# Kernel optimization log

Hardware: AMD Instinct MI355X
Metric: run time of the kernel (lower is better)

## Reference

```python
import jax, jax.numpy as jnp
import numpy as np
from jax import lax

B = 2; H = 32; W = 32; C = 384
NH = 12; NG = 6; KK = 7; STRIDE = 1; ORF = 2.0
CG = C // NG; HC = C // NH; GH = NH // NG; HID = 4 * C
EPS = 1e-5


def layernorm(x, w, b):
    mu = jnp.mean(x, axis=-1, keepdims=True)
    var = jnp.mean((x - mu) ** 2, axis=-1, keepdims=True)
    return (x - mu) * lax.rsqrt(var + EPS) * w + b


def ref_points(Hk, Wk):
    # normalized reference grid in (-1,1), ordering (y, x) as in _get_ref_points
    ry = ((jnp.arange(Hk, dtype=jnp.float32) + 0.5) / Hk) * 2.0 - 1.0
    rx = ((jnp.arange(Wk, dtype=jnp.float32) + 0.5) / Wk) * 2.0 - 1.0
    return jnp.stack(jnp.meshgrid(ry, rx, indexing='ij'), axis=-1)  # (Hk, Wk, 2)


def grid_sample(img, grid):
    # torch F.grid_sample: bilinear, align_corners=True, padding_mode='zeros'
    # img: (N, Cc, Hi, Wi); grid: (N, ..., 2) with (x, y) in [-1, 1]
    N, Cc, Hi, Wi = img.shape
    out_shape = grid.shape[1:-1]
    g = grid.reshape(N, -1, 2)
    x = (g[..., 0] + 1.0) * 0.5 * (Wi - 1)
    y = (g[..., 1] + 1.0) * 0.5 * (Hi - 1)
    x0 = jnp.floor(x); y0 = jnp.floor(y)
    wx1 = x - x0; wy1 = y - y0
    flat = img.reshape(N, Cc, Hi * Wi)
    M = g.shape[1]
    def gather(ix, iy, wgt):
        valid = (ix >= 0) & (ix <= Wi - 1) & (iy >= 0) & (iy <= Hi - 1)
        idx = (jnp.clip(iy, 0, Hi - 1) * Wi + jnp.clip(ix, 0, Wi - 1)).astype(jnp.int32)
        vals = jnp.take_along_axis(flat, jnp.broadcast_to(idx[:, None, :], (N, Cc, M)), axis=2)
        return vals * (wgt * valid.astype(img.dtype))[:, None, :]
    out = (gather(x0, y0, (1 - wx1) * (1 - wy1))
           + gather(x0 + 1, y0, wx1 * (1 - wy1))
           + gather(x0, y0 + 1, (1 - wx1) * wy1)
           + gather(x0 + 1, y0 + 1, wx1 * wy1))
    return out.reshape((N, Cc) + out_shape)


def setup_inputs() -> dict:
    ks = jax.random.split(jax.random.key(0), 16)
    n = lambda k, s, sc=0.02: jax.random.normal(k, s, jnp.float32) * sc
    return dict(
        x=jax.random.normal(ks[0], (B, H * W, C), jnp.float32),
        norm1_w=jnp.ones((C,), jnp.float32), norm1_b=jnp.zeros((C,), jnp.float32),
        wq=n(ks[1], (C, C)), bq=jnp.zeros((C,), jnp.float32),
        wk=n(ks[2], (C, C)), bk=jnp.zeros((C,), jnp.float32),
        wv=n(ks[3], (C, C)), bv=jnp.zeros((C,), jnp.float32),
        wo=n(ks[4], (C, C)), bo=jnp.zeros((C,), jnp.float32),
        off_dw_w=n(ks[5], (CG, 1, KK, KK)), off_dw_b=jnp.zeros((CG,), jnp.float32),
        off_ln_w=jnp.ones((CG,), jnp.float32), off_ln_b=jnp.zeros((CG,), jnp.float32),
        off_pw_w=n(ks[6], (2, CG)),
        rpe_table=n(ks[7], (NH, 2 * H - 1, 2 * W - 1), 0.01),
        norm2_w=jnp.ones((C,), jnp.float32), norm2_b=jnp.zeros((C,), jnp.float32),
        fc1_w=n(ks[8], (HID, C)), fc1_b=jnp.zeros((HID,), jnp.float32),
        fc2_w=n(ks[9], (C, HID)), fc2_b=jnp.zeros((C,), jnp.float32),
    )


def reference(x, norm1_w, norm1_b, wq, bq, wk, bk, wv, bv, wo, bo,
              off_dw_w, off_dw_b, off_ln_w, off_ln_b, off_pw_w, rpe_table,
              norm2_w, norm2_b, fc1_w, fc1_b, fc2_w, fc2_b):
    Bx, L, Cx = x.shape
    shortcut = x
    xn = layernorm(x, norm1_w, norm1_b)
    xi = xn.reshape(Bx, H, W, Cx).transpose(0, 3, 1, 2)  # (B, C, H, W)

    # proj_q (1x1 conv)
    q = jnp.einsum('bchw,dc->bdhw', xi, wq) + bq[None, :, None, None]

    # offset network on per-group channels
    q_off = q.reshape(Bx * NG, CG, H, W)
    o = lax.conv_general_dilated(q_off, off_dw_w, (STRIDE, STRIDE),
                                 [(KK // 2, KK // 2), (KK // 2, KK // 2)],
                                 dimension_numbers=('NCHW', 'OIHW', 'NCHW'),
                                 feature_group_count=CG) + off_dw_b[None, :, None, None]
    o = layernorm(o.transpose(0, 2, 3, 1), off_ln_w, off_ln_b)  # (Bg, Hk, Wk, CG)
    o = jax.nn.gelu(o, approximate=False)
    offset = jnp.einsum('bhwc,pc->bphw', o, off_pw_w)  # (Bg, 2, Hk, Wk)
    Hk, Wk = offset.shape[2], offset.shape[3]
    ns = Hk * Wk
    orange = jnp.array([1.0 / Hk, 1.0 / Wk], jnp.float32).reshape(1, 2, 1, 1)
    offset = jnp.tanh(offset) * orange * ORF
    offset = offset.transpose(0, 2, 3, 1)  # (Bg, Hk, Wk, 2) (y, x)
    pos = offset + ref_points(Hk, Wk)[None]  # offset_range_factor >= 0 branch

    # deformable sampling of the (normed) feature map
    xs = grid_sample(xi.reshape(Bx * NG, CG, H, W), pos[..., ::-1])  # (Bg, CG, Hk, Wk)
    xs = xs.reshape(Bx, Cx, 1, ns)

    k = (jnp.einsum('bcxn,dc->bdxn', xs, wk) + bk[None, :, None, None]).reshape(Bx * NH, HC, ns)
    v = (jnp.einsum('bcxn,dc->bdxn', xs, wv) + bv[None, :, None, None]).reshape(Bx * NH, HC, ns)
    q_ = q.reshape(Bx * NH, HC, H * W)

    attn = jnp.einsum('bcm,bcn->bmn', q_, k) * (HC ** -0.5)  # (B*NH, HW, ns)

    # continuous relative position bias via grid_sample on rpe_table
    rpe = jnp.broadcast_to(rpe_table[None], (Bx, NH, 2 * H - 1, 2 * W - 1)).reshape(
        Bx * NG, GH, 2 * H - 1, 2 * W - 1)
    qg = ref_points(H, W).reshape(H * W, 2)[None]  # (1, HW, 2)
    disp = (qg[:, :, None, :] - pos.reshape(Bx * NG, ns, 2)[:, None, :, :]) * 0.5  # (Bg, HW, ns, 2)
    bias = grid_sample(rpe, disp[..., ::-1])  # (Bg, GH, HW, ns)
    attn = attn + bias.reshape(Bx * NH, H * W, ns)

    attn = jax.nn.softmax(attn, axis=2)
    out = jnp.einsum('bmn,bcn->bcm', attn, v).reshape(Bx, Cx, H, W)
    y = jnp.einsum('bchw,dc->bdhw', out, wo) + bo[None, :, None, None]
    y = y.transpose(0, 2, 3, 1).reshape(Bx, L, Cx)

    x2 = shortcut + y
    h = layernorm(x2, norm2_w, norm2_b)
    h = jax.nn.gelu(h @ fc1_w.T + fc1_b, approximate=False) @ fc2_w.T + fc2_b
    return x2 + h
```

## Files before the change

kernel.cpp:

```cpp
#include <hip/hip_runtime.h>
#include <math.h>

#define Bc 2
#define Hh 32
#define Ww 32
#define Cc 384
#define NHc 12
#define NGc 6
#define CGc 64
#define HCc 32
#define GHc 2
#define HIDc 1536
#define Lc 1024
#define NSc 1024
#define BGc 12

typedef float f32x4 __attribute__((ext_vector_type(4)));
typedef short bf16x8 __attribute__((ext_vector_type(8)));

__device__ __forceinline__ float gelu_f(float v) {
    return 0.5f * v * (1.f + erff(v * 0.70710678118654752440f));
}

__device__ __forceinline__ unsigned short f2bf(float f) {
    unsigned u = __float_as_uint(f);
    u = (u + 0x7FFF + ((u >> 16) & 1)) >> 16;
    return (unsigned short)u;
}

__device__ __forceinline__ float bf2f(unsigned short u) {
    return __uint_as_float((unsigned)u << 16);
}

__global__ __launch_bounds__(128) void ln_kernel(
    const float* __restrict__ x, const float* __restrict__ w,
    const float* __restrict__ b, unsigned short* __restrict__ out)
{
    __shared__ float l1[2], l2[2];
    int row = blockIdx.x;
    int t = threadIdx.x;
    const float* xr = x + (size_t)row * Cc;
    float v0 = xr[t], v1 = xr[t + 128], v2 = xr[t + 256];
    float s = v0 + v1 + v2;
    #pragma unroll
    for (int o = 32; o; o >>= 1) s += __shfl_down(s, o);
    if ((t & 63) == 0) l1[t >> 6] = s;
    __syncthreads();
    float mu = (l1[0] + l1[1]) * (1.f / Cc);
    float d0 = v0 - mu, d1 = v1 - mu, d2 = v2 - mu;
    float q = d0 * d0 + d1 * d1 + d2 * d2;
    #pragma unroll
    for (int o = 32; o; o >>= 1) q += __shfl_down(q, o);
    if ((t & 63) == 0) l2[t >> 6] = q;
    __syncthreads();
    float rstd = rsqrtf((l2[0] + l2[1]) * (1.f / Cc) + 1e-5f);
    unsigned short* orow = out + (size_t)row * Cc;
    orow[t]       = f2bf(d0 * rstd * w[t]       + b[t]);
    orow[t + 128] = f2bf(d1 * rstd * w[t + 128] + b[t + 128]);
    orow[t + 256] = f2bf(d2 * rstd * w[t + 256] + b[t + 256]);
}

__global__ __launch_bounds__(256) void cast6_kernel(
    const float* __restrict__ wq, const float* __restrict__ wk,
    const float* __restrict__ wv, const float* __restrict__ wo,
    const float* __restrict__ f1, const float* __restrict__ f2,
    unsigned short* __restrict__ dq, unsigned short* __restrict__ dk,
    unsigned short* __restrict__ dv, unsigned short* __restrict__ d_o,
    unsigned short* __restrict__ d1, unsigned short* __restrict__ d2)
{
    int bid = blockIdx.x;
    const float* s; unsigned short* d; int base;
    if (bid < 144)       { s = wq; d = dq;  base = bid; }
    else if (bid < 288)  { s = wk; d = dk;  base = bid - 144; }
    else if (bid < 432)  { s = wv; d = dv;  base = bid - 288; }
    else if (bid < 576)  { s = wo; d = d_o; base = bid - 432; }
    else if (bid < 1152) { s = f1; d = d1;  base = bid - 576; }
    else                 { s = f2; d = d2;  base = bid - 1152; }
    int i = base * 1024 + threadIdx.x * 4;
    float4 v = *(const float4*)(s + i);
    ushort4 u;
    u.x = f2bf(v.x); u.y = f2bf(v.y); u.z = f2bf(v.z); u.w = f2bf(v.w);
    *(ushort4*)(d + i) = u;
}

template<int EPI>
__global__ __launch_bounds__(256) void mfma_gemm(
    const unsigned short* __restrict__ A, const unsigned short* __restrict__ W,
    const float* __restrict__ bias, const float* __restrict__ res,
    void* __restrict__ out1, void* __restrict__ out2, int M, int N, int K)
{
    int w = threadIdx.x >> 6, l = threadIdx.x & 63;
    int col = l & 15, quad = l >> 4;
    int mb = blockIdx.x * 64 + w * 16;
    int n0 = blockIdx.y * 32;
    const unsigned short* Ap = A + (size_t)(mb + col) * K + quad * 8;
    const unsigned short* Wp0 = W + (size_t)(n0 + col) * K + quad * 8;
    const unsigned short* Wp1 = W + (size_t)(n0 + 16 + col) * K + quad * 8;
    f32x4 acc[2] = {};
    #pragma unroll 4
    for (int k0 = 0; k0 < K; k0 += 32) {
        bf16x8 af = *(const bf16x8*)(Ap + k0);
        bf16x8 w0 = *(const bf16x8*)(Wp0 + k0);
        bf16x8 w1 = *(const bf16x8*)(Wp1 + k0);
        acc[0] = __builtin_amdgcn_mfma_f32_16x16x32_bf16(af, w0, acc[0], 0, 0, 0);
        acc[1] = __builtin_amdgcn_mfma_f32_16x16x32_bf16(af, w1, acc[1], 0, 0, 0);
    }
    int bb = mb >> 10, l0 = (mb & 1023) + quad * 4;
    #pragma unroll
    for (int ch = 0; ch < 2; ch++) {
        int n = n0 + ch * 16 + col;
        float bv = bias[n];
        if (EPI == 3) {
            unsigned short u0 = f2bf(acc[ch][0] + bv);
            unsigned short u1 = f2bf(acc[ch][1] + bv);
            unsigned short u2 = f2bf(acc[ch][2] + bv);
            unsigned short u3 = f2bf(acc[ch][3] + bv);
            ushort4 qv = {u0, u1, u2, u3};
            *(ushort4*)&((unsigned short*)out1)[((size_t)(bb * Cc + n)) * Lc + l0] = qv;
            unsigned short* q2 = (unsigned short*)out2;
            size_t base = (((size_t)(bb * NHc + (n >> 5))) * Lc + l0) * 32 + (n & 31);
            q2[base] = u0; q2[base + 32] = u1; q2[base + 64] = u2; q2[base + 96] = u3;
        } else {
            #pragma unroll
            for (int r = 0; r < 4; r++) {
                size_t m = mb + quad * 4 + r;
                float v = acc[ch][r] + bv;
                if (EPI == 1)
                    ((unsigned short*)out1)[m * N + n] = f2bf(gelu_f(v));
                else
                    ((float*)out1)[m * N + n] = v + res[m * N + n];
            }
        }
    }
}

__global__ __launch_bounds__(256) void mfma_kv(
    const unsigned short* __restrict__ A, const unsigned short* __restrict__ Wk,
    const unsigned short* __restrict__ Wv, const float* __restrict__ bk,
    const float* __restrict__ bv, unsigned short* __restrict__ kout,
    unsigned short* __restrict__ vout, int M, int K)
{
    int w = threadIdx.x >> 6, l = threadIdx.x & 63;
    int col = l & 15, quad = l >> 4;
    int mb = blockIdx.x * 64 + w * 16;
    int n0 = blockIdx.y * 32;
    const unsigned short* Ap = A + (size_t)(mb + col) * K + quad * 8;
    const unsigned short* Wk0 = Wk + (size_t)(n0 + col) * K + quad * 8;
    const unsigned short* Wk1 = Wk + (size_t)(n0 + 16 + col) * K + quad * 8;
    const unsigned short* Wv0 = Wv + (size_t)(n0 + col) * K + quad * 8;
    const unsigned short* Wv1 = Wv + (size_t)(n0 + 16 + col) * K + quad * 8;
    f32x4 ak[2] = {}, av[2] = {};
    #pragma unroll 4
    for (int k0 = 0; k0 < K; k0 += 32) {
        bf16x8 af = *(const bf16x8*)(Ap + k0);
        bf16x8 k0f = *(const bf16x8*)(Wk0 + k0);
        bf16x8 k1f = *(const bf16x8*)(Wk1 + k0);
        bf16x8 v0f = *(const bf16x8*)(Wv0 + k0);
        bf16x8 v1f = *(const bf16x8*)(Wv1 + k0);
        ak[0] = __builtin_amdgcn_mfma_f32_16x16x32_bf16(af, k0f, ak[0], 0, 0, 0);
        ak[1] = __builtin_amdgcn_mfma_f32_16x16x32_bf16(af, k1f, ak[1], 0, 0, 0);
        av[0] = __builtin_amdgcn_mfma_f32_16x16x32_bf16(af, v0f, av[0], 0, 0, 0);
        av[1] = __builtin_amdgcn_mfma_f32_16x16x32_bf16(af, v1f, av[1], 0, 0, 0);
    }
    int bb = mb >> 10, l0 = (mb & 1023) + quad * 4;
    #pragma unroll
    for (int ch = 0; ch < 2; ch++) {
        int n = n0 + ch * 16 + col;
        float bkv = bk[n], bvv = bv[n];
        #pragma unroll
        for (int r = 0; r < 4; r++)
            kout[(size_t)(mb + quad * 4 + r) * Cc + n] = f2bf(ak[ch][r] + bkv);
        ushort4 u;
        u.x = f2bf(av[ch][0] + bvv); u.y = f2bf(av[ch][1] + bvv);
        u.z = f2bf(av[ch][2] + bvv); u.w = f2bf(av[ch][3] + bvv);
        *(ushort4*)&vout[((size_t)(bb * Cc + n)) * NSc + l0] = u;
    }
}

__global__ __launch_bounds__(256) void dwconv_kernel(
    const unsigned short* __restrict__ q, const float* __restrict__ wdw,
    const float* __restrict__ bdw, float* __restrict__ o_dw)
{
    int cg = blockIdx.x, bg = blockIdx.y;
    int b = bg / NGc, g = bg % NGc;
    __shared__ float wk_s[49];
    __shared__ float img[1024];
    const unsigned short* qp = q + (size_t)(b * Cc + g * CGc + cg) * Lc;
    if (threadIdx.x < 49) wk_s[threadIdx.x] = wdw[cg * 49 + threadIdx.x];
    #pragma unroll
    for (int i = 0; i < 4; i++)
        img[threadIdx.x + i * 256] = bf2f(qp[threadIdx.x + i * 256]);
    __syncthreads();
    float bias = bdw[cg];
    #pragma unroll
    for (int i = 0; i < 4; i++) {
        int hw = threadIdx.x + i * 256;
        int y = hw >> 5, xx = hw & 31;
        float acc = bias;
        #pragma unroll
        for (int ky = 0; ky < 7; ky++) {
            int yy = y + ky - 3;
            if (yy < 0 || yy > 31) continue;
            #pragma unroll
            for (int kx = 0; kx < 7; kx++) {
                int x2 = xx + kx - 3;
                if (x2 < 0 || x2 > 31) continue;
                acc += img[yy * 32 + x2] * wk_s[ky * 7 + kx];
            }
        }
        o_dw[(size_t)(bg * CGc + cg) * Lc + hw] = acc;
    }
}

__global__ __launch_bounds__(256) void offset_kernel(
    const float* __restrict__ o_dw, const float* __restrict__ lnw,
    const float* __restrict__ lnb, const float* __restrict__ pw,
    float* __restrict__ pos)
{
    int hw = blockIdx.x * 4 + (threadIdx.x >> 6);
    int bg = blockIdx.y;
    int cg = threadIdx.x & 63;
    float v = o_dw[(size_t)(bg * CGc + cg) * Lc + hw];
    float s = v;
    #pragma unroll
    for (int o = 32; o; o >>= 1) s += __shfl_down(s, o);
    s = __shfl(s, 0, 64);
    float mu = s * (1.f / CGc);
    float d = v - mu;
    float q2 = d * d;
    #pragma unroll
    for (int o = 32; o; o >>= 1) q2 += __shfl_down(q2, o);
    q2 = __shfl(q2, 0, 64);
    float rstd = rsqrtf(q2 * (1.f / CGc) + 1e-5f);
    float t = d * rstd * lnw[cg] + lnb[cg];
    float gl = gelu_f(t);
    float sy = gl * pw[cg];
    float sx = gl * pw[CGc + cg];
    #pragma unroll
    for (int o = 32; o; o >>= 1) {
        sy += __shfl_down(sy, o);
        sx += __shfl_down(sx, o);
    }
    if (cg == 0) {
        float offy = tanhf(sy) * 0.0625f;
        float offx = tanhf(sx) * 0.0625f;
        int y = hw >> 5, xx = hw & 31;
        pos[((size_t)bg * Lc + hw) * 2 + 0] = offy + ((y + 0.5f) * (2.f / Hh) - 1.f);
        pos[((size_t)bg * Lc + hw) * 2 + 1] = offx + ((xx + 0.5f) * (2.f / Ww) - 1.f);
    }
}

__global__ __launch_bounds__(256) void sample_kernel(
    const unsigned short* __restrict__ xn, const float* __restrict__ pos,
    unsigned short* __restrict__ xs)
{
    int cg = threadIdx.x & 63;
    int nl = threadIdx.x >> 6;
    int n = blockIdx.x * 4 + nl;
    int bg = blockIdx.y;
    int b = bg / NGc, g = bg % NGc;
    float py = pos[((size_t)bg * NSc + n) * 2 + 0];
    float px = pos[((size_t)bg * NSc + n) * 2 + 1];
    float fx = (px + 1.f) * 0.5f * 31.f;
    float fy = (py + 1.f) * 0.5f * 31.f;
    float x0f = floorf(fx), y0f = floorf(fy);
    int x0 = (int)x0f, y0 = (int)y0f;
    float wx1 = fx - x0f, wy1 = fy - y0f;
    float wx0 = 1.f - wx1, wy0 = 1.f - wy1;
    const unsigned short* base = xn + (size_t)(b * Lc) * Cc + g * CGc + cg;
    float acc = 0.f;
    if (y0 >= 0 && y0 <= 31) {
        if (x0 >= 0 && x0 <= 31) acc += bf2f(base[(size_t)(y0 * 32 + x0) * Cc]) * wx0 * wy0;
        if (x0 + 1 >= 0 && x0 + 1 <= 31) acc += bf2f(base[(size_t)(y0 * 32 + x0 + 1) * Cc]) * wx1 * wy0;
    }
    if (y0 + 1 >= 0 && y0 + 1 <= 31) {
        if (x0 >= 0 && x0 <= 31) acc += bf2f(base[(size_t)((y0 + 1) * 32 + x0) * Cc]) * wx0 * wy1;
        if (x0 + 1 >= 0 && x0 + 1 <= 31) acc += bf2f(base[(size_t)((y0 + 1) * 32 + x0 + 1) * Cc]) * wx1 * wy1;
    }
    xs[((size_t)(b * NSc) + n) * Cc + g * CGc + cg] = f2bf(acc);
}

__global__ __launch_bounds__(256) void attn_kernel(
    const unsigned short* __restrict__ qbf, const unsigned short* __restrict__ kbf,
    const unsigned short* __restrict__ vtb, const float* __restrict__ pos,
    const float* __restrict__ rpe, unsigned short* __restrict__ attno)
{
    __shared__ float o_smem[2112];
    __shared__ unsigned short p_bf[4][16 * 72];
    __shared__ float ml_s[4][2][16];
    unsigned short* rpe_s = (unsigned short*)o_smem;

    int m0 = blockIdx.x * 16;
    int h = blockIdx.y, b = blockIdx.z;
    int tid = threadIdx.x;
    int w = tid >> 6, l = tid & 63;
    int col = l & 15, quad = l >> 4;

    const float* tb = rpe + (size_t)h * 3969;
    for (int i = tid; i < 63 * 65; i += 256) {
        int row = i / 65, cx = i - row * 65;
        rpe_s[i] = (cx < 63) ? f2bf(tb[row * 63 + cx] * 1.44269504f) : 0;
    }

    bf16x8 qfrag = *(const bf16x8*)(qbf +
        ((((size_t)(b * NHc + h)) * Lc + m0 + col) * 32 + quad * 8));

    float qgy = ((m0 >> 5) + 0.5f) * (2.f / 32.f) - 1.f;
    float qgx0 = (((m0 & 31) + quad * 4) + 0.5f) * (2.f / 32.f) - 1.f;

    const unsigned short* kb_ = kbf + (size_t)b * NSc * Cc + h * HCc;
    const unsigned short* vb_ = vtb + ((size_t)(b * Cc + h * HCc)) * NSc;
    const float2* pp = (const float2*)(pos + (size_t)(b * NGc + (h >> 1)) * NSc * 2);

    float run_m[4] = {-3.0e38f, -3.0e38f, -3.0e38f, -3.0e38f};
    float run_l[4] = {0.f, 0.f, 0.f, 0.f};
    f32x4 O0 = {0.f, 0.f, 0.f, 0.f};
    f32x4 O1 = {0.f, 0.f, 0.f, 0.f};

    __syncthreads();

    for (int it = 0; it < 4; it++) {
        int n0 = w * 256 + it * 64;
        f32x4 s[4];
        #pragma unroll
        for (int ch = 0; ch < 4; ch++) {
            bf16x8 kf = *(const bf16x8*)(kb_ +
                ((size_t)(n0 + ch * 16 + col) * Cc + quad * 8));
            f32x4 z = {0.f, 0.f, 0.f, 0.f};
            s[ch] = __builtin_amdgcn_mfma_f32_16x16x32_bf16(qfrag, kf, z, 0, 0, 0);
        }
        #pragma unroll
        for (int ch = 0; ch < 4; ch++) {
            int n = n0 + ch * 16 + col;
            float2 pyx = pp[n];
            float fy = ((qgy - pyx.x) * 0.5f + 1.f) * 31.f;
            float y0f = floorf(fy);
            int iy = (int)y0f;
            float wy1 = fy - y0f, wy0 = 1.f - wy1;
            bool y0ok = (unsigned)iy <= 62u;
            bool y1ok = (unsigned)(iy + 1) <= 62u;
            const unsigned short* r0 = rpe_s + iy * 65;
            float fx0 = ((qgx0 - pyx.y) * 0.5f + 1.f) * 31.f;
            #pragma unroll
            for (int r = 0; r < 4; r++) {
                float fx = fx0 + r * 0.96875f;
                float x0f = floorf(fx);
                int ix = (int)x0f;
                float wx1 = fx - x0f, wx0 = 1.f - wx1;
                bool x0ok = (unsigned)ix <= 62u;
                bool x1ok = (unsigned)(ix + 1) <= 62u;
                float bias = 0.f;
                if (y0ok) {
                    if (x0ok) bias += bf2f(r0[ix]) * wy0 * wx0;
                    if (x1ok) bias += bf2f(r0[ix + 1]) * wy0 * wx1;
                }
                if (y1ok) {
                    if (x0ok) bias += bf2f(r0[65 + ix]) * wy1 * wx0;
                    if (x1ok) bias += bf2f(r0[65 + ix + 1]) * wy1 * wx1;
                }
                s[ch][r] = s[ch][r] * 0.25506974f + bias;
            }
        }
        float nm[4], alpha[4];
        #pragma unroll
        for (int r = 0; r < 4; r++) {
            float mx = fmaxf(fmaxf(s[0][r], s[1][r]), fmaxf(s[2][r], s[3][r]));
            #pragma unroll
            for (int msk = 1; msk < 16; msk <<= 1)
                mx = fmaxf(mx, __shfl_xor(mx, msk));
            nm[r] = fmaxf(run_m[r], mx);
            alpha[r] = exp2f(run_m[r] - nm[r]);
            run_m[r] = nm[r];
        }
        float rowsum[4] = {0.f, 0.f, 0.f, 0.f};
        #pragma unroll
        for (int ch = 0; ch < 4; ch++)
            #pragma unroll
            for (int r = 0; r < 4; r++) {
                float e = exp2f(s[ch][r] - nm[r]);
                s[ch][r] = e;
                rowsum[r] += e;
            }
        #pragma unroll
        for (int r = 0; r < 4; r++) {
            float sm = rowsum[r];
            #pragma unroll
            for (int msk = 1; msk < 16; msk <<= 1)
                sm += __shfl_xor(sm, msk);
            run_l[r] = run_l[r] * alpha[r] + sm;
        }
        #pragma unroll
        for (int ch = 0; ch < 4; ch++)
            #pragma unroll
            for (int r = 0; r < 4; r++)
                p_bf[w][(quad * 4 + r) * 72 + ch * 16 + col] = f2bf(s[ch][r]);
        #pragma unroll
        for (int r = 0; r < 4; r++) { O0[r] *= alpha[r]; O1[r] *= alpha[r]; }
        #pragma unroll
        for (int half = 0; half < 2; half++) {
            bf16x8 pf = *(const bf16x8*)&p_bf[w][col * 72 + half * 32 + quad * 8];
            bf16x8 v0 = *(const bf16x8*)(vb_ +
                ((size_t)col * NSc + n0 + half * 32 + quad * 8));
            O0 = __builtin_amdgcn_mfma_f32_16x16x32_bf16(pf, v0, O0, 0, 0, 0);
            bf16x8 v1 = *(const bf16x8*)(vb_ +
                ((size_t)(col + 16) * NSc + n0 + half * 32 + quad * 8));
            O1 = __builtin_amdgcn_mfma_f32_16x16x32_bf16(pf, v1, O1, 0, 0, 0);
        }
    }
    __syncthreads();
    float* o_s = o_smem;
    #pragma unroll
    for (int r = 0; r < 4; r++) {
        int m = quad * 4 + r;
        o_s[w * 528 + m * 33 + col] = O0[r];
        o_s[w * 528 + m * 33 + col + 16] = O1[r];
    }
    if (col == 0) {
        #pragma unroll
        for (int r = 0; r < 4; r++) {
            ml_s[w][0][quad * 4 + r] = run_m[r];
            ml_s[w][1][quad * 4 + r] = run_l[r];
        }
    }
    __syncthreads();
    for (int i = tid; i < 512; i += 256) {
        int m = i >> 5, c = i & 31;
        float fm = fmaxf(fmaxf(ml_s[0][0][m], ml_s[1][0][m]),
                         fmaxf(ml_s[2][0][m], ml_s[3][0][m]));
        float lsum = 0.f, osum = 0.f;
        #pragma unroll
        for (int ww = 0; ww < 4; ww++) {
            float sc = exp2f(ml_s[ww][0][m] - fm);
            lsum += ml_s[ww][1][m] * sc;
            osum += o_s[ww * 528 + m * 33 + c] * sc;
        }
        attno[((size_t)(b * Lc) + m0 + m) * Cc + h * HCc + c] = f2bf(osum / lsum);
    }
}

extern "C" void kernel_launch(void* const* d_in, const int* in_sizes, int n_in,
                              void* d_out, int out_size, void* d_ws, size_t ws_size,
                              hipStream_t stream)
{
    const float* x    = (const float*)d_in[0];
    const float* n1w  = (const float*)d_in[1];
    const float* n1b  = (const float*)d_in[2];
    const float* wq   = (const float*)d_in[3];
    const float* bq   = (const float*)d_in[4];
    const float* wk   = (const float*)d_in[5];
    const float* bk   = (const float*)d_in[6];
    const float* wv   = (const float*)d_in[7];
    const float* bv   = (const float*)d_in[8];
    const float* wo   = (const float*)d_in[9];
    const float* bo   = (const float*)d_in[10];
    const float* dw_w = (const float*)d_in[11];
    const float* dw_b = (const float*)d_in[12];
    const float* lnw  = (const float*)d_in[13];
    const float* lnb  = (const float*)d_in[14];
    const float* pw_w = (const float*)d_in[15];
    const float* rpe  = (const float*)d_in[16];
    const float* n2w  = (const float*)d_in[17];
    const float* n2b  = (const float*)d_in[18];
    const float* fc1w = (const float*)d_in[19];
    const float* fc1b = (const float*)d_in[20];
    const float* fc2w = (const float*)d_in[21];
    const float* fc2b = (const float*)d_in[22];
    float* out = (float*)d_out;

    float* ws = (float*)d_ws;
    unsigned short* xnbf = (unsigned short*)ws;
    unsigned short* qb16 = (unsigned short*)(ws + 393216);
    unsigned short* qbf  = (unsigned short*)(ws + 1179648);
    unsigned short* h1bf = (unsigned short*)ws;
    float* odw   = ws + 1572864;
    unsigned short* xln2bf = (unsigned short*)(ws + 1572864);
    float* posb  = ws + 2359296;
    unsigned short* xsbf = (unsigned short*)(ws + 2383872);
    unsigned short* kbf  = (unsigned short*)(ws + 2777088);
    unsigned short* vtb  = (unsigned short*)(ws + 3170304);
    unsigned short* attnbf = (unsigned short*)(ws + 3563520);
    float* x2    = ws + 3956736;
    unsigned short* wqbf   = (unsigned short*)(ws + 4743168);
    unsigned short* wkbf   = (unsigned short*)(ws + 4816896);
    unsigned short* wvbf   = (unsigned short*)(ws + 4890624);
    unsigned short* wobf   = (unsigned short*)(ws + 4964352);
    unsigned short* fc1wbf = (unsigned short*)(ws + 5038080);
    unsigned short* fc2wbf = (unsigned short*)(ws + 5332992);

    cast6_kernel<<<1728, 256, 0, stream>>>(
        wq, wk, wv, wo, fc1w, fc2w, wqbf, wkbf, wvbf, wobf, fc1wbf, fc2wbf);
    ln_kernel<<<Bc * Lc, 128, 0, stream>>>(x, n1w, n1b, xnbf);
    mfma_gemm<3><<<dim3(Bc * Lc / 64, Cc / 32), 256, 0, stream>>>(
        xnbf, wqbf, bq, x, qb16, qbf, Bc * Lc, Cc, Cc);
    dwconv_kernel<<<dim3(CGc, BGc), 256, 0, stream>>>(qb16, dw_w, dw_b, odw);
    offset_kernel<<<dim3(Lc / 4, BGc), 256, 0, stream>>>(odw, lnw, lnb, pw_w, posb);
    sample_kernel<<<dim3(NSc / 4, BGc), 256, 0, stream>>>(xnbf, posb, xsbf);
    mfma_kv<<<dim3(Bc * NSc / 64, Cc / 32), 256, 0, stream>>>(
        xsbf, wkbf, wvbf, bk, bv, kbf, vtb, Bc * NSc, Cc);
    attn_kernel<<<dim3(Lc / 16, NHc, Bc), 256, 0, stream>>>(
        qbf, kbf, vtb, posb, rpe, attnbf);
    mfma_gemm<2><<<dim3(Bc * Lc / 64, Cc / 32), 256, 0, stream>>>(
        attnbf, wobf, bo, x, x2, x2, Bc * Lc, Cc, Cc);
    ln_kernel<<<Bc * Lc, 128, 0, stream>>>(x2, n2w, n2b, xln2bf);
    mfma_gemm<1><<<dim3(Bc * Lc / 64, HIDc / 32), 256, 0, stream>>>(
        xln2bf, fc1wbf, fc1b, x2, h1bf, h1bf, Bc * Lc, HIDc, Cc);
    mfma_gemm<2><<<dim3(Bc * Lc / 64, Cc / 32), 256, 0, stream>>>(
        h1bf, fc2wbf, fc2b, x2, out, out, Bc * Lc, Cc, HIDc);
}
```

Measured before the change: 297.8 us.

## Split attention key range across two blocks and merge partials in new kernel

The attention kernel now splits the 1024 sampled keys into two halves, each handled by a separate block, which doubles the grid from 1536 to 3072 blocks. Each block writes an unnormalized partial output in bf16 plus per-row max and sum, and a new merge kernel combines the two halves with log-sum-exp rescaling. The aim is more parallelism and better occupancy on the many-CU GPU. In exchange, every block reloads the rpe table into shared memory, there is an extra launch, and partial outputs pass through global memory. Storing the unnormalized partials in bf16 also adds rounding error.

```diff
diff --git a/kernel.cpp b/kernel.cpp
--- a/kernel.cpp
+++ b/kernel.cpp
@@ -283,7 +283,8 @@
 __global__ __launch_bounds__(256) void attn_kernel(
     const unsigned short* __restrict__ qbf, const unsigned short* __restrict__ kbf,
     const unsigned short* __restrict__ vtb, const float* __restrict__ pos,
-    const float* __restrict__ rpe, unsigned short* __restrict__ attno)
+    const float* __restrict__ rpe, unsigned short* __restrict__ pO,
+    float* __restrict__ pML)
 {
     __shared__ float o_smem[2112];
     __shared__ unsigned short p_bf[4][16 * 72];
@@ -291,7 +292,8 @@
     unsigned short* rpe_s = (unsigned short*)o_smem;
 
     int m0 = blockIdx.x * 16;
-    int h = blockIdx.y, b = blockIdx.z;
+    int h = blockIdx.y >> 1, half = blockIdx.y & 1;
+    int b = blockIdx.z;
     int tid = threadIdx.x;
     int w = tid >> 6, l = tid & 63;
     int col = l & 15, quad = l >> 4;
@@ -319,8 +321,8 @@
 
     __syncthreads();
 
-    for (int it = 0; it < 4; it++) {
-        int n0 = w * 256 + it * 64;
+    for (int it = 0; it < 2; it++) {
+        int n0 = half * 512 + w * 128 + it * 64;
         f32x4 s[4];
         #pragma unroll
         for (int ch = 0; ch < 4; ch++) {
@@ -397,13 +399,13 @@
         #pragma unroll
         for (int r = 0; r < 4; r++) { O0[r] *= alpha[r]; O1[r] *= alpha[r]; }
         #pragma unroll
-        for (int half = 0; half < 2; half++) {
-            bf16x8 pf = *(const bf16x8*)&p_bf[w][col * 72 + half * 32 + quad * 8];
+        for (int halfn = 0; halfn < 2; halfn++) {
+            bf16x8 pf = *(const bf16x8*)&p_bf[w][col * 72 + halfn * 32 + quad * 8];
             bf16x8 v0 = *(const bf16x8*)(vb_ +
-                ((size_t)col * NSc + n0 + half * 32 + quad * 8));
+                ((size_t)col * NSc + n0 + halfn * 32 + quad * 8));
             O0 = __builtin_amdgcn_mfma_f32_16x16x32_bf16(pf, v0, O0, 0, 0, 0);
             bf16x8 v1 = *(const bf16x8*)(vb_ +
-                ((size_t)(col + 16) * NSc + n0 + half * 32 + quad * 8));
+                ((size_t)(col + 16) * NSc + n0 + halfn * 32 + quad * 8));
             O1 = __builtin_amdgcn_mfma_f32_16x16x32_bf16(pf, v1, O1, 0, 0, 0);
         }
     }
@@ -423,6 +425,7 @@
         }
     }
     __syncthreads();
+    size_t tile = (((size_t)(b * NHc + h) * 64) + blockIdx.x) * 2 + half;
     for (int i = tid; i < 512; i += 256) {
         int m = i >> 5, c = i & 31;
         float fm = fmaxf(fmaxf(ml_s[0][0][m], ml_s[1][0][m]),
@@ -434,7 +437,30 @@
             lsum += ml_s[ww][1][m] * sc;
             osum += o_s[ww * 528 + m * 33 + c] * sc;
         }
-        attno[((size_t)(b * Lc) + m0 + m) * Cc + h * HCc + c] = f2bf(osum / lsum);
+        pO[tile * 512 + i] = f2bf(osum);
+        if (c == 0) {
+            pML[tile * 32 + m * 2]     = fm;
+            pML[tile * 32 + m * 2 + 1] = lsum;
+        }
+    }
+}
+
+__global__ __launch_bounds__(256) void attn_merge(
+    const unsigned short* __restrict__ pO, const float* __restrict__ pML,
+    unsigned short* __restrict__ attno)
+{
+    int mt = blockIdx.x, h = blockIdx.y, b = blockIdx.z;
+    size_t tile0 = (((size_t)(b * NHc + h) * 64) + mt) * 2;
+    int tid = threadIdx.x;
+    for (int i = tid; i < 512; i += 256) {
+        int m = i >> 5, c = i & 31;
+        float m0v = pML[tile0 * 32 + m * 2], l0 = pML[tile0 * 32 + m * 2 + 1];
+        float m1v = pML[(tile0 + 1) * 32 + m * 2], l1 = pML[(tile0 + 1) * 32 + m * 2 + 1];
+        float M = fmaxf(m0v, m1v);
+        float s0 = exp2f(m0v - M), s1 = exp2f(m1v - M);
+        float lsum = l0 * s0 + l1 * s1;
+        float o = bf2f(pO[tile0 * 512 + i]) * s0 + bf2f(pO[(tile0 + 1) * 512 + i]) * s1;
+        attno[((size_t)(b * Lc) + mt * 16 + m) * Cc + h * HCc + c] = f2bf(o / lsum);
     }
 }
 
@@ -472,6 +498,8 @@
     unsigned short* qb16 = (unsigned short*)(ws + 393216);
     unsigned short* qbf  = (unsigned short*)(ws + 1179648);
     unsigned short* h1bf = (unsigned short*)ws;
+    unsigned short* pO   = (unsigned short*)ws;
+    float*          pML  = ws + 786432;
     float* odw   = ws + 1572864;
     unsigned short* xln2bf = (unsigned short*)(ws + 1572864);
     float* posb  = ws + 2359296;
@@ -497,8 +525,9 @@
     sample_kernel<<<dim3(NSc / 4, BGc), 256, 0, stream>>>(xnbf, posb, xsbf);
     mfma_kv<<<dim3(Bc * NSc / 64, Cc / 32), 256, 0, stream>>>(
         xsbf, wkbf, wvbf, bk, bv, kbf, vtb, Bc * NSc, Cc);
-    attn_kernel<<<dim3(Lc / 16, NHc, Bc), 256, 0, stream>>>(
-        qbf, kbf, vtb, posb, rpe, attnbf);
+    attn_kernel<<<dim3(Lc / 16, NHc * 2, Bc), 256, 0, stream>>>(
+        qbf, kbf, vtb, posb, rpe, pO, pML);
+    attn_merge<<<dim3(Lc / 16, NHc, Bc), 256, 0, stream>>>(pO, pML, attnbf);
     mfma_gemm<2><<<dim3(Bc * Lc / 64, Cc / 32), 256, 0, stream>>>(
         attnbf, wobf, bo, x, x2, x2, Bc * Lc, Cc, Cc);
     ln_kernel<<<Bc * Lc, 128, 0, stream>>>(x2, n2w, n2b, xln2bf);
```

Result: no change. 303.6 us (+2.0%).
